# Performance work log

Measured on AMD Instinct MI355X. Metric: run time of the kernel, lower is better.

The kernel has to match this reference:

```python
import jax, jax.numpy as jnp
import numpy as np

IN_CH = 512
OUT_CH = 512
HEADS = 8
HEAD_DIM = OUT_CH // HEADS
N = 64 * 64  # total flattened tokens


def setup_inputs() -> dict:
    key = jax.random.key(0)
    ks = jax.random.split(key, 10)
    x = jax.random.normal(ks[0], (64, 64, IN_CH), dtype=jnp.float32)
    edge_index = jax.random.randint(ks[1], (2, 65536), 0, N, dtype=jnp.int64)
    # causal temporal mask, broadcastable against scores [N, H, N]
    temporal_mask = jnp.tril(jnp.ones((N, N), dtype=bool))[:, None, :]
    s = 1.0 / np.sqrt(IN_CH)
    Wq = jax.random.uniform(ks[2], (OUT_CH, IN_CH), minval=-s, maxval=s)
    bq = jnp.zeros((OUT_CH,), jnp.float32)
    Wk = jax.random.uniform(ks[3], (OUT_CH, IN_CH), minval=-s, maxval=s)
    bk = jnp.zeros((OUT_CH,), jnp.float32)
    Wv = jax.random.uniform(ks[4], (OUT_CH, IN_CH), minval=-s, maxval=s)
    bv = jnp.zeros((OUT_CH,), jnp.float32)
    Wo = jax.random.uniform(ks[5], (OUT_CH, OUT_CH), minval=-s, maxval=s)
    bo = jnp.zeros((OUT_CH,), jnp.float32)
    return {"x": x, "edge_index": edge_index, "temporal_mask": temporal_mask,
            "Wq": Wq, "bq": bq, "Wk": Wk, "bk": bk, "Wv": Wv, "bv": bv,
            "Wo": Wo, "bo": bo}


def reference(x, edge_index, temporal_mask, Wq, bq, Wk, bk, Wv, bv, Wo, bo):
    # x: [S1, S2, C] -> flatten to [N, C]; edge_index unused (as in source).
    xf = x.reshape(-1, IN_CH)
    q = (xf @ Wq.T + bq).reshape(-1, HEADS, HEAD_DIM)
    k = (xf @ Wk.T + bk).reshape(-1, HEADS, HEAD_DIM)
    v = (xf @ Wv.T + bv).reshape(-1, HEADS, HEAD_DIM)
    scores = jnp.einsum('nhd,mhd->nhm', q, k) / np.sqrt(HEAD_DIM)  # [N,H,N]
    scores = jnp.where(temporal_mask, scores, -jnp.inf)
    attn = jax.nn.softmax(scores, axis=-1)  # dropout omitted (eval mode)
    out = jnp.einsum('nhm,mhd->nhd', attn, v).reshape(-1, OUT_CH)
    return out @ Wo.T + bo  # [N, OUT_CH]
```

## Files before the change

kernel.cpp:

```cpp
#include <hip/hip_runtime.h>
#include <math.h>

#define NT 4096
#define CH 512
#define NHEADS 8
#define HD 64

typedef __attribute__((ext_vector_type(8))) short short8;
typedef __attribute__((ext_vector_type(4))) float f32x4;
typedef unsigned short ushort_t;
typedef unsigned int uint_t;

#define MFMA16 __builtin_amdgcn_mfma_f32_16x16x32_bf16

#define MNEG 1e30f

__device__ __forceinline__ ushort_t f2bf(float x) {
  uint_t u = __float_as_uint(x);
  return (ushort_t)((u + 0x7fffu + ((u >> 16) & 1u)) >> 16);
}
__device__ __forceinline__ float bf2f(ushort_t h) {
  return __uint_as_float(((uint_t)h) << 16);
}

__device__ __forceinline__ void g2l16(const ushort_t* g, ushort_t* l) {
  __builtin_amdgcn_global_load_lds(
      (const __attribute__((address_space(1))) void*)g,
      (__attribute__((address_space(3))) void*)l, 16, 0, 0);
}

__device__ __forceinline__ short8 ldsFrag(const ushort_t* plane, int row, int c4) {
  return *reinterpret_cast<const short8*>(plane + row * 64 + (((c4) ^ (row & 7)) << 3));
}

__global__ __launch_bounds__(256)
void cvt_hi(const float* __restrict__ x,
            const float* __restrict__ Wq, const float* __restrict__ Wk,
            const float* __restrict__ Wv, const float* __restrict__ Wo,
            ushort_t* __restrict__ xh, ushort_t* __restrict__ qh,
            ushort_t* __restrict__ kh, ushort_t* __restrict__ vh,
            ushort_t* __restrict__ oh) {
  const size_t i = ((size_t)blockIdx.x * 256 + threadIdx.x) * 4;
  const float* src;
  ushort_t* dh;
  size_t off;
  if (i < 2097152) { src = x; dh = xh; off = i; }
  else {
    const size_t j = i - 2097152;
    const int wsel = (int)(j >> 18);
    off = j & 262143;
    if (wsel == 0)      { src = Wq; dh = qh; }
    else if (wsel == 1) { src = Wk; dh = kh; }
    else if (wsel == 2) { src = Wv; dh = vh; }
    else                { src = Wo; dh = oh; }
  }
  const float4 v = *reinterpret_cast<const float4*>(src + off);
  const ushort_t hb[4] = {f2bf(v.x), f2bf(v.y), f2bf(v.z), f2bf(v.w)};
  *reinterpret_cast<uint2*>(dh + off) =
      make_uint2((uint_t)hb[0] | ((uint_t)hb[1] << 16), (uint_t)hb[2] | ((uint_t)hb[3] << 16));
}

__device__ __forceinline__ void gemm_hi_core(
    const ushort_t* __restrict__ Ah, const ushort_t* __restrict__ Wh,
    int m0, int n0, int w, int lane, ushort_t* ldsA, ushort_t* ldsW,
    f32x4 acc[2][4]) {
  const int l15 = lane & 15;
  const int g = lane >> 4;
  for (int k0 = 0; k0 < 512; k0 += 64) {
    __syncthreads();
    #pragma unroll
    for (int p = 0; p < 4; ++p) {
      const int c = 256 * p + 64 * w + lane;
      const int r = c >> 3;
      const int sc4 = (c & 7) ^ (r & 7);
      g2l16(Ah + (size_t)(m0 + r) * 512 + k0 + sc4 * 8, &ldsA[(256 * p + 64 * w) * 8]);
    }
    #pragma unroll
    for (int p = 0; p < 2; ++p) {
      const int c = 256 * p + 64 * w + lane;
      const int r = c >> 3;
      const int sc4 = (c & 7) ^ (r & 7);
      g2l16(Wh + (size_t)(n0 + r) * 512 + k0 + sc4 * 8, &ldsW[(256 * p + 64 * w) * 8]);
    }
    __syncthreads();
    #pragma unroll
    for (int s = 0; s < 2; ++s) {
      short8 ah[2];
      #pragma unroll
      for (int mt = 0; mt < 2; ++mt)
        ah[mt] = ldsFrag(ldsA, 32 * w + 16 * mt + l15, 4 * s + g);
      #pragma unroll
      for (int nt = 0; nt < 4; ++nt) {
        const short8 wh = ldsFrag(ldsW, 16 * nt + l15, 4 * s + g);
        #pragma unroll
        for (int mt = 0; mt < 2; ++mt)
          acc[mt][nt] = MFMA16(ah[mt], wh, acc[mt][nt], 0, 0, 0);
      }
    }
  }
}

__global__ __launch_bounds__(256)
void gemm_qkv_bf16(const ushort_t* __restrict__ xh,
                   const ushort_t* __restrict__ Wqh, const float* __restrict__ bq,
                   const ushort_t* __restrict__ Wkh, const float* __restrict__ bk,
                   const ushort_t* __restrict__ Wvh, const float* __restrict__ bv,
                   ushort_t* __restrict__ Qhi, ushort_t* __restrict__ Khi,
                   ushort_t* __restrict__ Vthi) {
  __shared__ ushort_t ldsA[128 * 64];
  __shared__ ushort_t ldsW[64 * 64];
  const int z = blockIdx.z;
  const ushort_t* Wh = (z == 0) ? Wqh : (z == 1) ? Wkh : Wvh;
  const float* bias = (z == 0) ? bq : (z == 1) ? bk : bv;

  const int t = threadIdx.x;
  const int w = t >> 6;
  const int lane = t & 63;
  const int l15 = lane & 15;
  const int g = lane >> 4;
  const int m0 = blockIdx.x * 128;
  const int n0 = blockIdx.y * 64;

  f32x4 acc[2][4];
  #pragma unroll
  for (int mt = 0; mt < 2; ++mt)
    #pragma unroll
    for (int nt = 0; nt < 4; ++nt) acc[mt][nt] = f32x4{0.f, 0.f, 0.f, 0.f};

  gemm_hi_core(xh, Wh, m0, n0, w, lane, ldsA, ldsW, acc);

  if (z < 2) {
    ushort_t* Hi = z ? Khi : Qhi;
    const float sc = z ? 1.0f : 0.125f;
    #pragma unroll
    for (int mt = 0; mt < 2; ++mt) {
      const int mb = m0 + 32 * w + 16 * mt + 4 * g;
      #pragma unroll
      for (int nt = 0; nt < 4; ++nt) {
        const int col = n0 + 16 * nt + l15;
        const float bv_ = bias[col];
        #pragma unroll
        for (int r = 0; r < 4; ++r)
          Hi[(size_t)(mb + r) * 512 + col] = f2bf((acc[mt][nt][r] + bv_) * sc);
      }
    }
  } else {
    #pragma unroll
    for (int mt = 0; mt < 2; ++mt) {
      const int mb = m0 + 32 * w + 16 * mt + 4 * g;
      #pragma unroll
      for (int nt = 0; nt < 4; ++nt) {
        const int n = n0 + 16 * nt + l15;
        const float bv_ = bias[n];
        ushort_t hb[4];
        #pragma unroll
        for (int r = 0; r < 4; ++r) hb[r] = f2bf(acc[mt][nt][r] + bv_);
        *reinterpret_cast<uint2*>(&Vthi[(size_t)n * 4096 + mb]) =
            make_uint2((uint_t)hb[0] | ((uint_t)hb[1] << 16),
                       (uint_t)hb[2] | ((uint_t)hb[3] << 16));
      }
    }
  }
}

__global__ __launch_bounds__(256)
void gemm_out_bf16(const ushort_t* __restrict__ Ahi, const ushort_t* __restrict__ Woh,
                   const float* __restrict__ bias, float* __restrict__ C) {
  __shared__ ushort_t ldsA[128 * 64];
  __shared__ ushort_t ldsW[64 * 64];
  const int t = threadIdx.x;
  const int w = t >> 6;
  const int lane = t & 63;
  const int l15 = lane & 15;
  const int g = lane >> 4;
  const int m0 = blockIdx.x * 128;
  const int n0 = blockIdx.y * 64;

  f32x4 acc[2][4];
  #pragma unroll
  for (int mt = 0; mt < 2; ++mt)
    #pragma unroll
    for (int nt = 0; nt < 4; ++nt) acc[mt][nt] = f32x4{0.f, 0.f, 0.f, 0.f};

  gemm_hi_core(Ahi, Woh, m0, n0, w, lane, ldsA, ldsW, acc);

  #pragma unroll
  for (int mt = 0; mt < 2; ++mt) {
    const int mb = m0 + 32 * w + 16 * mt + 4 * g;
    #pragma unroll
    for (int nt = 0; nt < 4; ++nt) {
      const int col = n0 + 16 * nt + l15;
      const float bv_ = bias[col];
      #pragma unroll
      for (int r = 0; r < 4; ++r)
        C[(size_t)(mb + r) * 512 + col] = acc[mt][nt][r] + bv_;
    }
  }
}

__global__ __launch_bounds__(512)
void attn_mfma(const ushort_t* __restrict__ Qhi, const ushort_t* __restrict__ Khi,
               const ushort_t* __restrict__ Vthi,
               float* __restrict__ Opart, float2* __restrict__ MLpart) {
  __shared__ ushort_t ldsK[2][64 * 64];
  __shared__ ushort_t ldsV[2][64 * 64];
  __shared__ ushort_t ldsP[8][16 * 64];

  const int t = threadIdx.x;
  const int h = blockIdx.y;
  const int w = t >> 6;
  const int lane = t & 63;
  const int l15 = lane & 15;
  const int g = lane >> 4;

  const int bx = blockIdx.x;
  const int qb = 31 - bx / 3;
  const int sp = bx - 3 * (bx / 3);
  const int ntp = qb + 1;
  const int len = (ntp + 2) / 3;
  const int pb0 = sp * len;
  const int pb1e = (pb0 + len < ntp) ? (pb0 + len) : ntp;
  const int q0 = qb * 128;
  const int qr = q0 + w * 16 + l15;

  const short8 ones = {(short)0x3F80, (short)0x3F80, (short)0x3F80, (short)0x3F80,
                       (short)0x3F80, (short)0x3F80, (short)0x3F80, (short)0x3F80};

  short8 qh[2];
  #pragma unroll
  for (int s = 0; s < 2; ++s)
    qh[s] = *reinterpret_cast<const short8*>(
        Qhi + (size_t)qr * 512 + h * 64 + 32 * s + 8 * g);

  float mrun[4], lrun[4];
  f32x4 accO[4];
  #pragma unroll
  for (int r = 0; r < 4; ++r) { mrun[r] = -MNEG; lrun[r] = 0.f; }
  #pragma unroll
  for (int dt = 0; dt < 4; ++dt) accO[dt] = f32x4{0.f, 0.f, 0.f, 0.f};

  for (int pair = pb0; pair < pb1e; ++pair) {
    __syncthreads();
    {
      const int c = w * 64 + lane;
      const int r = c >> 3;
      const int sc4 = (c & 7) ^ (r & 7);
      const int ldst = (w * 64) * 8;
      const int kt0 = 2 * pair, kt1 = 2 * pair + 1;
      g2l16(Khi + (size_t)(kt0 * 64 + r) * 512 + h * 64 + sc4 * 8, &ldsK[0][ldst]);
      g2l16(Khi + (size_t)(kt1 * 64 + r) * 512 + h * 64 + sc4 * 8, &ldsK[1][ldst]);
      g2l16(Vthi + (size_t)(h * 64 + r) * 4096 + kt0 * 64 + sc4 * 8, &ldsV[0][ldst]);
      g2l16(Vthi + (size_t)(h * 64 + r) * 4096 + kt1 * 64 + sc4 * 8, &ldsV[1][ldst]);
    }
    __syncthreads();

    #pragma unroll
    for (int st = 0; st < 2; ++st) {
      const int kt = 2 * pair + st;

      f32x4 accS[4];
      #pragma unroll
      for (int nt = 0; nt < 4; ++nt) accS[nt] = f32x4{0.f, 0.f, 0.f, 0.f};
      __builtin_amdgcn_s_setprio(1);
      #pragma unroll
      for (int s = 0; s < 2; ++s) {
        #pragma unroll
        for (int nt = 0; nt < 4; ++nt) {
          const short8 kh = ldsFrag(ldsK[st], 16 * nt + l15, 4 * s + g);
          accS[nt] = MFMA16(qh[s], kh, accS[nt], 0, 0, 0);
        }
      }
      __builtin_amdgcn_s_setprio(0);

      if (pair == qb) {
        #pragma unroll
        for (int nt = 0; nt < 4; ++nt) {
          const int kg = kt * 64 + 16 * nt + l15;
          #pragma unroll
          for (int r = 0; r < 4; ++r) {
            const int qg = q0 + w * 16 + 4 * g + r;
            if (kg > qg) accS[nt][r] = -INFINITY;
          }
        }
      }

      float pmax[4];
      #pragma unroll
      for (int r = 0; r < 4; ++r)
        pmax[r] = fmaxf(fmaxf(accS[0][r], accS[1][r]), fmaxf(accS[2][r], accS[3][r]));
      float dd = pmax[0] - mrun[0];
      #pragma unroll
      for (int r = 1; r < 4; ++r) dd = fmaxf(dd, pmax[r] - mrun[r]);
      if (!__all(dd <= 8.0f)) {
        #pragma unroll
        for (int off = 1; off < 16; off <<= 1)
          #pragma unroll
          for (int r = 0; r < 4; ++r) pmax[r] = fmaxf(pmax[r], __shfl_xor(pmax[r], off));
        #pragma unroll
        for (int r = 0; r < 4; ++r) {
          const float mn = fmaxf(mrun[r], pmax[r]);
          const float al = __expf(mrun[r] - mn);
          mrun[r] = mn;
          lrun[r] *= al;
          #pragma unroll
          for (int dt = 0; dt < 4; ++dt) accO[dt][r] *= al;
        }
      }
      #pragma unroll
      for (int nt = 0; nt < 4; ++nt)
        #pragma unroll
        for (int r = 0; r < 4; ++r) {
          const float p = __expf(accS[nt][r] - mrun[r]);
          const int row = 4 * g + r;
          ldsP[w][row * 64 + (((2 * nt + (l15 >> 3)) ^ (row & 7)) << 3) + (l15 & 7)]
              = f2bf(p);
        }
      short8 pah[2];
      #pragma unroll
      for (int s = 0; s < 2; ++s) pah[s] = ldsFrag(ldsP[w], l15, 4 * s + g);

      f32x4 accL = f32x4{0.f, 0.f, 0.f, 0.f};
      __builtin_amdgcn_s_setprio(1);
      #pragma unroll
      for (int s = 0; s < 2; ++s) {
        accL = MFMA16(pah[s], ones, accL, 0, 0, 0);
        #pragma unroll
        for (int dt = 0; dt < 4; ++dt) {
          const short8 vh = ldsFrag(ldsV[st], 16 * dt + l15, 4 * s + g);
          accO[dt] = MFMA16(pah[s], vh, accO[dt], 0, 0, 0);
        }
      }
      __builtin_amdgcn_s_setprio(0);
      #pragma unroll
      for (int r = 0; r < 4; ++r) lrun[r] += accL[r];
    }
  }

  #pragma unroll
  for (int r = 0; r < 4; ++r) {
    const int rw = w * 16 + 4 * g + r;
    const size_t pbase = ((((size_t)sp * 32 + qb) * 8 + h) * 128 + rw) * 64;
    #pragma unroll
    for (int dt = 0; dt < 4; ++dt)
      Opart[pbase + 16 * dt + l15] = accO[dt][r];
    if (l15 == 0)
      MLpart[(((size_t)sp * 32 + qb) * 8 + h) * 128 + rw] = make_float2(mrun[r], lrun[r]);
  }
}

__global__ __launch_bounds__(512)
void attn_combine(const float* __restrict__ Opart, const float2* __restrict__ MLpart,
                  ushort_t* __restrict__ Ahi) {
  const int qb = blockIdx.x;
  const int h = blockIdx.y;
  const int t = threadIdx.x;
  const int row = t >> 2;
  const int c0 = (t & 3) * 16;
  const size_t mlidx = (((size_t)qb) * 8 + h) * 128 + row;
  const size_t SPS = (size_t)32 * 8 * 128;
  const float2 ml0 = MLpart[mlidx];
  const float2 ml1 = MLpart[mlidx + SPS];
  const float2 ml2 = MLpart[mlidx + 2 * SPS];
  const float M = fmaxf(fmaxf(ml0.x, ml1.x), ml2.x);
  const float w0 = __expf(ml0.x - M);
  const float w1 = __expf(ml1.x - M);
  const float w2 = __expf(ml2.x - M);
  const float inv = 1.0f / (w0 * ml0.y + w1 * ml1.y + w2 * ml2.y);
  const size_t b0 = mlidx * 64;
  const size_t b1 = (mlidx + SPS) * 64;
  const size_t b2 = (mlidx + 2 * SPS) * 64;
  #pragma unroll
  for (int p = 0; p < 4; ++p) {
    const int col = c0 + p * 4;
    const float4 o0 = *reinterpret_cast<const float4*>(&Opart[b0 + col]);
    const float4 o1 = *reinterpret_cast<const float4*>(&Opart[b1 + col]);
    const float4 o2 = *reinterpret_cast<const float4*>(&Opart[b2 + col]);
    ushort_t hb[4];
    hb[0] = f2bf((o0.x * w0 + o1.x * w1 + o2.x * w2) * inv);
    hb[1] = f2bf((o0.y * w0 + o1.y * w1 + o2.y * w2) * inv);
    hb[2] = f2bf((o0.z * w0 + o1.z * w1 + o2.z * w2) * inv);
    hb[3] = f2bf((o0.w * w0 + o1.w * w1 + o2.w * w2) * inv);
    const size_t idx = (size_t)(qb * 128 + row) * 512 + h * 64 + col;
    *reinterpret_cast<uint2*>(&Ahi[idx]) =
        make_uint2((uint_t)hb[0] | ((uint_t)hb[1] << 16), (uint_t)hb[2] | ((uint_t)hb[3] << 16));
  }
}

extern "C" void kernel_launch(void* const* d_in, const int* in_sizes, int n_in,
                              void* d_out, int out_size, void* d_ws, size_t ws_size,
                              hipStream_t stream) {
  const float* x  = (const float*)d_in[0];
  const float* Wq = (const float*)d_in[3];
  const float* bq = (const float*)d_in[4];
  const float* Wk = (const float*)d_in[5];
  const float* bk = (const float*)d_in[6];
  const float* Wv = (const float*)d_in[7];
  const float* bv = (const float*)d_in[8];
  const float* Wo = (const float*)d_in[9];
  const float* bo = (const float*)d_in[10];
  float* out = (float*)d_out;

  ushort_t* p = (ushort_t*)d_ws;
  const size_t NC = (size_t)NT * CH;
  const size_t WW = (size_t)CH * CH;
  ushort_t* xhi = p;            p += NC;
  ushort_t* Wqh = p;            p += WW;
  ushort_t* Wkh = p;            p += WW;
  ushort_t* Wvh = p;            p += WW;
  ushort_t* Woh = p;            p += WW;
  ushort_t* Qhi = p;            p += NC;
  ushort_t* Khi = p;            p += NC;
  ushort_t* Vthi = p;           p += NC;
  ushort_t* Ahi = p;            p += NC;
  float* Opart = (float*)p;
  float2* MLpart = (float2*)(Opart + 6291456);

  cvt_hi<<<3072, 256, 0, stream>>>(x, Wq, Wk, Wv, Wo, xhi, Wqh, Wkh, Wvh, Woh);
  gemm_qkv_bf16<<<dim3(32, 8, 3), 256, 0, stream>>>(
      xhi, Wqh, bq, Wkh, bk, Wvh, bv, Qhi, Khi, Vthi);
  attn_mfma<<<dim3(96, 8), 512, 0, stream>>>(Qhi, Khi, Vthi, Opart, MLpart);
  attn_combine<<<dim3(32, 8), 512, 0, stream>>>(Opart, MLpart, Ahi);
  gemm_out_bf16<<<dim3(32, 8), 256, 0, stream>>>(Ahi, Woh, bo, out);
}
```

Baseline: 91.55 us.

## Replace fixed 3-way split attention grid with persistent atomic work queue

```diff
diff --git a/kernel.cpp b/kernel.cpp
--- a/kernel.cpp
+++ b/kernel.cpp
@@ -198,153 +198,166 @@
   }
 }
 
+#define NITEMS 640
+
 __global__ __launch_bounds__(512)
-void attn_mfma(const ushort_t* __restrict__ Qhi, const ushort_t* __restrict__ Khi,
-               const ushort_t* __restrict__ Vthi,
-               float* __restrict__ Opart, float2* __restrict__ MLpart) {
+void attn_persist(const ushort_t* __restrict__ Qhi, const ushort_t* __restrict__ Khi,
+                  const ushort_t* __restrict__ Vthi,
+                  float* __restrict__ Opart, float2* __restrict__ MLpart,
+                  int* __restrict__ ctr) {
   __shared__ ushort_t ldsK[2][64 * 64];
   __shared__ ushort_t ldsV[2][64 * 64];
   __shared__ ushort_t ldsP[8][16 * 64];
+  __shared__ int s_item;
 
   const int t = threadIdx.x;
-  const int h = blockIdx.y;
   const int w = t >> 6;
   const int lane = t & 63;
   const int l15 = lane & 15;
   const int g = lane >> 4;
 
-  const int bx = blockIdx.x;
-  const int qb = 31 - bx / 3;
-  const int sp = bx - 3 * (bx / 3);
-  const int ntp = qb + 1;
-  const int len = (ntp + 2) / 3;
-  const int pb0 = sp * len;
-  const int pb1e = (pb0 + len < ntp) ? (pb0 + len) : ntp;
-  const int q0 = qb * 128;
-  const int qr = q0 + w * 16 + l15;
-
   const short8 ones = {(short)0x3F80, (short)0x3F80, (short)0x3F80, (short)0x3F80,
                        (short)0x3F80, (short)0x3F80, (short)0x3F80, (short)0x3F80};
 
-  short8 qh[2];
-  #pragma unroll
-  for (int s = 0; s < 2; ++s)
-    qh[s] = *reinterpret_cast<const short8*>(
-        Qhi + (size_t)qr * 512 + h * 64 + 32 * s + 8 * g);
-
-  float mrun[4], lrun[4];
-  f32x4 accO[4];
-  #pragma unroll
-  for (int r = 0; r < 4; ++r) { mrun[r] = -MNEG; lrun[r] = 0.f; }
-  #pragma unroll
-  for (int dt = 0; dt < 4; ++dt) accO[dt] = f32x4{0.f, 0.f, 0.f, 0.f};
-
-  for (int pair = pb0; pair < pb1e; ++pair) {
+  for (;;) {
     __syncthreads();
-    {
-      const int c = w * 64 + lane;
-      const int r = c >> 3;
-      const int sc4 = (c & 7) ^ (r & 7);
-      const int ldst = (w * 64) * 8;
-      const int kt0 = 2 * pair, kt1 = 2 * pair + 1;
-      g2l16(Khi + (size_t)(kt0 * 64 + r) * 512 + h * 64 + sc4 * 8, &ldsK[0][ldst]);
-      g2l16(Khi + (size_t)(kt1 * 64 + r) * 512 + h * 64 + sc4 * 8, &ldsK[1][ldst]);
-      g2l16(Vthi + (size_t)(h * 64 + r) * 4096 + kt0 * 64 + sc4 * 8, &ldsV[0][ldst]);
-      g2l16(Vthi + (size_t)(h * 64 + r) * 4096 + kt1 * 64 + sc4 * 8, &ldsV[1][ldst]);
-    }
+    if (t == 0) s_item = atomicAdd(ctr, 1);
     __syncthreads();
-
-    #pragma unroll
-    for (int st = 0; st < 2; ++st) {
-      const int kt = 2 * pair + st;
-
-      f32x4 accS[4];
-      #pragma unroll
-      for (int nt = 0; nt < 4; ++nt) accS[nt] = f32x4{0.f, 0.f, 0.f, 0.f};
-      __builtin_amdgcn_s_setprio(1);
-      #pragma unroll
-      for (int s = 0; s < 2; ++s) {
-        #pragma unroll
-        for (int nt = 0; nt < 4; ++nt) {
-          const short8 kh = ldsFrag(ldsK[st], 16 * nt + l15, 4 * s + g);
-          accS[nt] = MFMA16(qh[s], kh, accS[nt], 0, 0, 0);
-        }
+    const int it = s_item;
+    if (it >= NITEMS) break;
+
+    const int h = it & 7;
+    const int cid = it >> 3;
+    int qb, ch;
+    if (cid < 32)      { qb = 31 - (cid >> 2); ch = cid & 3; }
+    else if (cid < 56) { const int j = cid - 32; qb = 23 - j / 3; ch = j - 3 * (j / 3); }
+    else if (cid < 72) { const int j = cid - 56; qb = 15 - (j >> 1); ch = j & 1; }
+    else               { qb = 7 - (cid - 72); ch = 0; }
+    const int pb0 = ch * 8;
+    const int pb1e = (pb0 + 8 < qb + 1) ? (pb0 + 8) : (qb + 1);
+    const int q0 = qb * 128;
+    const int qr = q0 + w * 16 + l15;
+
+    short8 qh[2];
+    #pragma unroll
+    for (int s = 0; s < 2; ++s)
+      qh[s] = *reinterpret_cast<const short8*>(
+          Qhi + (size_t)qr * 512 + h * 64 + 32 * s + 8 * g);
+
+    float mrun[4], lrun[4];
+    f32x4 accO[4];
+    #pragma unroll
+    for (int r = 0; r < 4; ++r) { mrun[r] = -MNEG; lrun[r] = 0.f; }
+    #pragma unroll
+    for (int dt = 0; dt < 4; ++dt) accO[dt] = f32x4{0.f, 0.f, 0.f, 0.f};
+
+    for (int pair = pb0; pair < pb1e; ++pair) {
+      __syncthreads();
+      {
+        const int c = w * 64 + lane;
+        const int r = c >> 3;
+        const int sc4 = (c & 7) ^ (r & 7);
+        const int ldst = (w * 64) * 8;
+        const int kt0 = 2 * pair, kt1 = 2 * pair + 1;
+        g2l16(Khi + (size_t)(kt0 * 64 + r) * 512 + h * 64 + sc4 * 8, &ldsK[0][ldst]);
+        g2l16(Khi + (size_t)(kt1 * 64 + r) * 512 + h * 64 + sc4 * 8, &ldsK[1][ldst]);
+        g2l16(Vthi + (size_t)(h * 64 + r) * 4096 + kt0 * 64 + sc4 * 8, &ldsV[0][ldst]);
+        g2l16(Vthi + (size_t)(h * 64 + r) * 4096 + kt1 * 64 + sc4 * 8, &ldsV[1][ldst]);
       }
-      __builtin_amdgcn_s_setprio(0);
-
-      if (pair == qb) {
-        #pragma unroll
-        for (int nt = 0; nt < 4; ++nt) {
-          const int kg = kt * 64 + 16 * nt + l15;
-          #pragma unroll
-          for (int r = 0; r < 4; ++r) {
-            const int qg = q0 + w * 16 + 4 * g + r;
-            if (kg > qg) accS[nt][r] = -INFINITY;
+      __syncthreads();
+
+      #pragma unroll
+      for (int st = 0; st < 2; ++st) {
+        const int kt = 2 * pair + st;
+
+        f32x4 accS[4];
+        #pragma unroll
+        for (int nt = 0; nt < 4; ++nt) accS[nt] = f32x4{0.f, 0.f, 0.f, 0.f};
+        __builtin_amdgcn_s_setprio(1);
+        #pragma unroll
+        for (int s = 0; s < 2; ++s) {
+          #pragma unroll
+          for (int nt = 0; nt < 4; ++nt) {
+            const short8 kh = ldsFrag(ldsK[st], 16 * nt + l15, 4 * s + g);
+            accS[nt] = MFMA16(qh[s], kh, accS[nt], 0, 0, 0);
           }
         }
+        __builtin_amdgcn_s_setprio(0);
+
+        if (pair == qb) {
+          #pragma unroll
+          for (int nt = 0; nt < 4; ++nt) {
+            const int kg = kt * 64 + 16 * nt + l15;
+            #pragma unroll
+            for (int r = 0; r < 4; ++r) {
+              const int qg = q0 + w * 16 + 4 * g + r;
+              if (kg > qg) accS[nt][r] = -INFINITY;
+            }
+          }
+        }
+
+        float pmax[4];
+        #pragma unroll
+        for (int r = 0; r < 4; ++r)
+          pmax[r] = fmaxf(fmaxf(accS[0][r], accS[1][r]), fmaxf(accS[2][r], accS[3][r]));
+        float dd = pmax[0] - mrun[0];
+        #pragma unroll
+        for (int r = 1; r < 4; ++r) dd = fmaxf(dd, pmax[r] - mrun[r]);
+        if (!__all(dd <= 8.0f)) {
+          #pragma unroll
+          for (int off = 1; off < 16; off <<= 1)
+            #pragma unroll
+            for (int r = 0; r < 4; ++r) pmax[r] = fmaxf(pmax[r], __shfl_xor(pmax[r], off));
+          #pragma unroll
+          for (int r = 0; r < 4; ++r) {
+            const float mn = fmaxf(mrun[r], pmax[r]);
+            const float al = __expf(mrun[r] - mn);
+            mrun[r] = mn;
+            lrun[r] *= al;
+            #pragma unroll
+            for (int dt = 0; dt < 4; ++dt) accO[dt][r] *= al;
+          }
+        }
+        #pragma unroll
+        for (int nt = 0; nt < 4; ++nt)
+          #pragma unroll
+          for (int r = 0; r < 4; ++r) {
+            const float p = __expf(accS[nt][r] - mrun[r]);
+            const int row = 4 * g + r;
+            ldsP[w][row * 64 + (((2 * nt + (l15 >> 3)) ^ (row & 7)) << 3) + (l15 & 7)]
+                = f2bf(p);
+          }
+        short8 pah[2];
+        #pragma unroll
+        for (int s = 0; s < 2; ++s) pah[s] = ldsFrag(ldsP[w], l15, 4 * s + g);
+
+        f32x4 accL = f32x4{0.f, 0.f, 0.f, 0.f};
+        __builtin_amdgcn_s_setprio(1);
+        #pragma unroll
+        for (int s = 0; s < 2; ++s) {
+          accL = MFMA16(pah[s], ones, accL, 0, 0, 0);
+          #pragma unroll
+          for (int dt = 0; dt < 4; ++dt) {
+            const short8 vh = ldsFrag(ldsV[st], 16 * dt + l15, 4 * s + g);
+            accO[dt] = MFMA16(pah[s], vh, accO[dt], 0, 0, 0);
+          }
+        }
+        __builtin_amdgcn_s_setprio(0);
+        #pragma unroll
+        for (int r = 0; r < 4; ++r) lrun[r] += accL[r];
       }
-
-      float pmax[4];
-      #pragma unroll
-      for (int r = 0; r < 4; ++r)
-        pmax[r] = fmaxf(fmaxf(accS[0][r], accS[1][r]), fmaxf(accS[2][r], accS[3][r]));
-      float dd = pmax[0] - mrun[0];
-      #pragma unroll
-      for (int r = 1; r < 4; ++r) dd = fmaxf(dd, pmax[r] - mrun[r]);
-      if (!__all(dd <= 8.0f)) {
-        #pragma unroll
-        for (int off = 1; off < 16; off <<= 1)
-          #pragma unroll
-          for (int r = 0; r < 4; ++r) pmax[r] = fmaxf(pmax[r], __shfl_xor(pmax[r], off));
-        #pragma unroll
-        for (int r = 0; r < 4; ++r) {
-          const float mn = fmaxf(mrun[r], pmax[r]);
-          const float al = __expf(mrun[r] - mn);
-          mrun[r] = mn;
-          lrun[r] *= al;
-          #pragma unroll
-          for (int dt = 0; dt < 4; ++dt) accO[dt][r] *= al;
-        }
-      }
-      #pragma unroll
-      for (int nt = 0; nt < 4; ++nt)
-        #pragma unroll
-        for (int r = 0; r < 4; ++r) {
-          const float p = __expf(accS[nt][r] - mrun[r]);
-          const int row = 4 * g + r;
-          ldsP[w][row * 64 + (((2 * nt + (l15 >> 3)) ^ (row & 7)) << 3) + (l15 & 7)]
-              = f2bf(p);
-        }
-      short8 pah[2];
-      #pragma unroll
-      for (int s = 0; s < 2; ++s) pah[s] = ldsFrag(ldsP[w], l15, 4 * s + g);
-
-      f32x4 accL = f32x4{0.f, 0.f, 0.f, 0.f};
-      __builtin_amdgcn_s_setprio(1);
-      #pragma unroll
-      for (int s = 0; s < 2; ++s) {
-        accL = MFMA16(pah[s], ones, accL, 0, 0, 0);
-        #pragma unroll
-        for (int dt = 0; dt < 4; ++dt) {
-          const short8 vh = ldsFrag(ldsV[st], 16 * dt + l15, 4 * s + g);
-          accO[dt] = MFMA16(pah[s], vh, accO[dt], 0, 0, 0);
-        }
-      }
-      __builtin_amdgcn_s_setprio(0);
-      #pragma unroll
-      for (int r = 0; r < 4; ++r) lrun[r] += accL[r];
-    }
-  }
-
-  #pragma unroll
-  for (int r = 0; r < 4; ++r) {
-    const int rw = w * 16 + 4 * g + r;
-    const size_t pbase = ((((size_t)sp * 32 + qb) * 8 + h) * 128 + rw) * 64;
-    #pragma unroll
-    for (int dt = 0; dt < 4; ++dt)
-      Opart[pbase + 16 * dt + l15] = accO[dt][r];
-    if (l15 == 0)
-      MLpart[(((size_t)sp * 32 + qb) * 8 + h) * 128 + rw] = make_float2(mrun[r], lrun[r]);
+    }
+
+    #pragma unroll
+    for (int r = 0; r < 4; ++r) {
+      const int rw = w * 16 + 4 * g + r;
+      const size_t pbase = ((((size_t)ch * 32 + qb) * 8 + h) * 128 + rw) * 64;
+      #pragma unroll
+      for (int dt = 0; dt < 4; ++dt)
+        Opart[pbase + 16 * dt + l15] = accO[dt][r];
+      if (l15 == 0)
+        MLpart[(((size_t)ch * 32 + qb) * 8 + h) * 128 + rw] = make_float2(mrun[r], lrun[r]);
+    }
   }
 }
 
@@ -356,30 +369,38 @@
   const int t = threadIdx.x;
   const int row = t >> 2;
   const int c0 = (t & 3) * 16;
+  const int nch = (qb + 8) / 8;
   const size_t mlidx = (((size_t)qb) * 8 + h) * 128 + row;
   const size_t SPS = (size_t)32 * 8 * 128;
-  const float2 ml0 = MLpart[mlidx];
-  const float2 ml1 = MLpart[mlidx + SPS];
-  const float2 ml2 = MLpart[mlidx + 2 * SPS];
-  const float M = fmaxf(fmaxf(ml0.x, ml1.x), ml2.x);
-  const float w0 = __expf(ml0.x - M);
-  const float w1 = __expf(ml1.x - M);
-  const float w2 = __expf(ml2.x - M);
-  const float inv = 1.0f / (w0 * ml0.y + w1 * ml1.y + w2 * ml2.y);
-  const size_t b0 = mlidx * 64;
-  const size_t b1 = (mlidx + SPS) * 64;
-  const size_t b2 = (mlidx + 2 * SPS) * 64;
+
+  float M = -MNEG;
+  float2 ml[4];
+  for (int s = 0; s < nch; ++s) {
+    ml[s] = MLpart[mlidx + (size_t)s * SPS];
+    M = fmaxf(M, ml[s].x);
+  }
+  float ww[4];
+  float l = 0.f;
+  for (int s = 0; s < nch; ++s) {
+    ww[s] = __expf(ml[s].x - M);
+    l += ww[s] * ml[s].y;
+  }
+  const float inv = 1.0f / l;
+
   #pragma unroll
   for (int p = 0; p < 4; ++p) {
     const int col = c0 + p * 4;
-    const float4 o0 = *reinterpret_cast<const float4*>(&Opart[b0 + col]);
-    const float4 o1 = *reinterpret_cast<const float4*>(&Opart[b1 + col]);
-    const float4 o2 = *reinterpret_cast<const float4*>(&Opart[b2 + col]);
+    float f0 = 0.f, f1 = 0.f, f2 = 0.f, f3 = 0.f;
+    for (int s = 0; s < nch; ++s) {
+      const float4 o = *reinterpret_cast<const float4*>(
+          &Opart[(mlidx + (size_t)s * SPS) * 64 + col]);
+      f0 += o.x * ww[s]; f1 += o.y * ww[s]; f2 += o.z * ww[s]; f3 += o.w * ww[s];
+    }
     ushort_t hb[4];
-    hb[0] = f2bf((o0.x * w0 + o1.x * w1 + o2.x * w2) * inv);
-    hb[1] = f2bf((o0.y * w0 + o1.y * w1 + o2.y * w2) * inv);
-    hb[2] = f2bf((o0.z * w0 + o1.z * w1 + o2.z * w2) * inv);
-    hb[3] = f2bf((o0.w * w0 + o1.w * w1 + o2.w * w2) * inv);
+    hb[0] = f2bf(f0 * inv);
+    hb[1] = f2bf(f1 * inv);
+    hb[2] = f2bf(f2 * inv);
+    hb[3] = f2bf(f3 * inv);
     const size_t idx = (size_t)(qb * 128 + row) * 512 + h * 64 + col;
     *reinterpret_cast<uint2*>(&Ahi[idx]) =
         make_uint2((uint_t)hb[0] | ((uint_t)hb[1] << 16), (uint_t)hb[2] | ((uint_t)hb[3] << 16));
@@ -413,12 +434,14 @@
   ushort_t* Vthi = p;           p += NC;
   ushort_t* Ahi = p;            p += NC;
   float* Opart = (float*)p;
-  float2* MLpart = (float2*)(Opart + 6291456);
-
+  float2* MLpart = (float2*)(Opart + 8388608);
+  int* ctr = (int*)(MLpart + 131072);
+
+  hipMemsetAsync(ctr, 0, 4, stream);
   cvt_hi<<<3072, 256, 0, stream>>>(x, Wq, Wk, Wv, Wo, xhi, Wqh, Wkh, Wvh, Woh);
   gemm_qkv_bf16<<<dim3(32, 8, 3), 256, 0, stream>>>(
       xhi, Wqh, bq, Wkh, bk, Wvh, bv, Qhi, Khi, Vthi);
-  attn_mfma<<<dim3(96, 8), 512, 0, stream>>>(Qhi, Khi, Vthi, Opart, MLpart);
+  attn_persist<<<768, 512, 0, stream>>>(Qhi, Khi, Vthi, Opart, MLpart, ctr);
   attn_combine<<<dim3(32, 8), 512, 0, stream>>>(Opart, MLpart, Ahi);
   gemm_out_bf16<<<dim3(32, 8), 256, 0, stream>>>(Ahi, Woh, bo, out);
 }
```

Result: slower. 125.2 us (+36.7%).
